# Kernel optimization log

Hardware: AMD Instinct MI355X
Metric: run time of the kernel (lower is better)

## Reference

```python
import jax, jax.numpy as jnp
import numpy as np

MARGIN = 1.0   # TripletLoss(margin) init arg
EPS = 1e-6     # torch F.pairwise_distance eps used by nn.TripletMarginLoss
INF = 1e9

N, D_EMB, N_CLASSES = 8192, 1024, 128


def setup_inputs() -> dict:
    key = jax.random.key(0)
    k1, k2 = jax.random.split(key)
    embeddings = jax.random.normal(k1, (N, D_EMB), dtype=jnp.float32)
    target = jax.random.randint(k2, (N,), 0, N_CLASSES, dtype=jnp.int64 if jax.config.jax_enable_x64 else jnp.int32)
    return {"embeddings": embeddings, "target": target}


def _mine_and_loss(embeddings, target):
    # Vectorized, deterministic equivalent of the per-anchor random mining loop:
    # full pairwise L2 distance matrix via a GEMM (compute-bound core).
    sq = jnp.sum(embeddings * embeddings, axis=1)                      # [N]
    d2 = sq[:, None] + sq[None, :] - 2.0 * (embeddings @ embeddings.T)  # [N, N]
    Dm = jnp.sqrt(jnp.maximum(d2, 0.0))                                 # [N, N]

    same = target[:, None] == target[None, :]
    eye = jnp.eye(target.shape[0], dtype=bool)
    pos_mask = same & ~eye          # valid positives (same class, not self)
    neg_mask = ~same                # valid negatives (different class)

    # Positive: hardest (farthest) same-class sample (deterministic stand-in
    # for the original's random positive draw).
    pos_scores = jnp.where(pos_mask, Dm, -INF)
    pos_idx = jnp.argmax(pos_scores, axis=1)                           # [N]
    d_p = jnp.max(pos_scores, axis=1)                                  # [N]

    # Negative: semi-hard (d_p < d_n < d_p + margin), pick the closest such
    # negative; if none exists, fall back to the overall hardest (min-dist)
    # negative -- mirrors the loop's early-break vs. min_dist fallback.
    semi = neg_mask & (Dm > d_p[:, None]) & (Dm < (d_p + MARGIN)[:, None])
    has_semi = jnp.any(semi, axis=1)
    neg_semi = jnp.argmin(jnp.where(semi, Dm, INF), axis=1)
    neg_hard = jnp.argmin(jnp.where(neg_mask, Dm, INF), axis=1)
    neg_idx = jnp.where(has_semi, neg_semi, neg_hard)                  # [N]

    # nn.TripletMarginLoss(margin, p=2): mean(relu(d(a,p) - d(a,n) + margin))
    # with torch's pairwise_distance eps added to the difference.
    a = embeddings
    p = embeddings[pos_idx]
    n = embeddings[neg_idx]
    dp = jnp.sqrt(jnp.sum((a - p + EPS) ** 2, axis=1))
    dn = jnp.sqrt(jnp.sum((a - n + EPS) ** 2, axis=1))
    return jnp.mean(jax.nn.relu(dp - dn + MARGIN))


def reference(embeddings, target):
    return _mine_and_loss(embeddings, target)
```

## Files before the change

kernel.cpp:

```cpp
#include <hip/hip_runtime.h>
#include <hip/hip_bf16.h>

#define N 8192
#define D 1024
#define MARGIN 1.0f
#define EPS 1e-6f

typedef __attribute__((ext_vector_type(8))) short bf16x8;
typedef __attribute__((ext_vector_type(4))) float f32x4;
typedef __attribute__((ext_vector_type(8))) _Float16 f16x8;
typedef __attribute__((ext_vector_type(4))) _Float16 f16x4;
typedef __attribute__((ext_vector_type(8))) unsigned short u16x8;

__device__ inline unsigned short f2bf(float x) {
    unsigned u = __float_as_uint(x);
    unsigned r = (u + 0x7FFFu + ((u >> 16) & 1u)) >> 16;
    return (unsigned short)r;
}

__device__ inline float h2f(unsigned hb) {
    return (float)__builtin_bit_cast(_Float16, (unsigned short)hb);
}

__global__ __launch_bounds__(256) void prep_kernel(const float* __restrict__ E,
                                                   unsigned short* __restrict__ Ebf,
                                                   float* __restrict__ sq) {
    const int r = blockIdx.x;
    const int tid = threadIdx.x;
    const float4 v = ((const float4*)(E + (size_t)r * D))[tid];
    ushort4 o;
    o.x = f2bf(v.x); o.y = f2bf(v.y); o.z = f2bf(v.z); o.w = f2bf(v.w);
    ((ushort4*)(Ebf + (size_t)r * D))[tid] = o;
    float s = v.x * v.x + v.y * v.y + v.z * v.z + v.w * v.w;
    for (int off = 32; off > 0; off >>= 1) s += __shfl_down(s, off);
    __shared__ float red[4];
    const int lane = tid & 63, wave = tid >> 6;
    if (lane == 0) red[wave] = s;
    __syncthreads();
    if (tid == 0) sq[r] = red[0] + red[1] + red[2] + red[3];
}

__global__ __launch_bounds__(256) void cls_kernel(const int* __restrict__ target,
                                                  unsigned char* __restrict__ cls) {
    const int t = blockIdx.x * 256 + threadIdx.x;
    cls[t] = (unsigned char)target[t];
}

__global__ __launch_bounds__(256) void gemm_kernel(const unsigned short* __restrict__ E,
                                                   const float* __restrict__ sq,
                                                   _Float16* __restrict__ D2h) {
    __shared__ char smem[128 * 136 * 2];
    unsigned short* As = (unsigned short*)smem;
    unsigned short* Bs = (unsigned short*)(smem + 8192);
    _Float16* Ts = (_Float16*)smem;

    const int tid = threadIdx.x;
    const int lane = tid & 63;
    const int wave = tid >> 6;
    const int wm = wave & 1, wn = wave >> 1;

    const int l = blockIdx.x;
    int by = (int)((sqrtf(8.0f * (float)l + 1.0f) - 1.0f) * 0.5f);
    while ((by + 1) * (by + 2) / 2 <= l) ++by;
    while (by * (by + 1) / 2 > l) --by;
    const int bx = l - by * (by + 1) / 2;
    const int rm = by * 128;
    const int cn = bx * 128;

    const int srow = tid >> 2;
    const int scol = (tid & 3) * 8;

    const unsigned short* gA = E + (size_t)(rm + srow) * D + scol;
    const unsigned short* gB = E + (size_t)(cn + srow) * D + scol;

    f32x4 acc[4][4] = {};

    const int kq = (lane >> 4) * 8;
    const int mr = lane & 15;

    for (int k0 = 0; k0 < D; k0 += 32) {
        __builtin_amdgcn_global_load_lds(
            (const __attribute__((address_space(1))) unsigned int*)(gA + k0),
            (__attribute__((address_space(3))) unsigned int*)((char*)As + wave * 1024), 16, 0, 0);
        __builtin_amdgcn_global_load_lds(
            (const __attribute__((address_space(1))) unsigned int*)(gA + (size_t)64 * D + k0),
            (__attribute__((address_space(3))) unsigned int*)((char*)As + 4096 + wave * 1024), 16, 0, 0);
        __builtin_amdgcn_global_load_lds(
            (const __attribute__((address_space(1))) unsigned int*)(gB + k0),
            (__attribute__((address_space(3))) unsigned int*)((char*)Bs + wave * 1024), 16, 0, 0);
        __builtin_amdgcn_global_load_lds(
            (const __attribute__((address_space(1))) unsigned int*)(gB + (size_t)64 * D + k0),
            (__attribute__((address_space(3))) unsigned int*)((char*)Bs + 4096 + wave * 1024), 16, 0, 0);
        __syncthreads();

        bf16x8 af[4], bfr[4];
#pragma unroll
        for (int mi = 0; mi < 4; ++mi)
            af[mi] = *(const bf16x8*)(As + (wm * 64 + mi * 16 + mr) * 32 + kq);
#pragma unroll
        for (int ni = 0; ni < 4; ++ni)
            bfr[ni] = *(const bf16x8*)(Bs + (wn * 64 + ni * 16 + mr) * 32 + kq);
#pragma unroll
        for (int mi = 0; mi < 4; ++mi)
#pragma unroll
            for (int ni = 0; ni < 4; ++ni)
                acc[mi][ni] = __builtin_amdgcn_mfma_f32_16x16x32_bf16(af[mi], bfr[ni], acc[mi][ni], 0, 0, 0);
        __syncthreads();
    }

    const int crow = (lane >> 4) * 4;
    const int ccol = lane & 15;
    const bool offdiag = (bx != by);
    float sqj[4];
#pragma unroll
    for (int ni = 0; ni < 4; ++ni)
        sqj[ni] = sq[cn + wn * 64 + ni * 16 + ccol];
#pragma unroll
    for (int mi = 0; mi < 4; ++mi) {
        const int lrow = wm * 64 + mi * 16 + crow;
        const int i0 = rm + lrow;
        float sqi[4];
#pragma unroll
        for (int r = 0; r < 4; ++r) sqi[r] = sq[i0 + r];
#pragma unroll
        for (int ni = 0; ni < 4; ++ni) {
            const int lcol = wn * 64 + ni * 16 + ccol;
            const int j = cn + lcol;
            f16x4 tv;
#pragma unroll
            for (int r = 0; r < 4; ++r) {
                float d2 = fmaxf(sqi[r] + sqj[ni] - 2.0f * acc[mi][ni][r], 0.0f);
                _Float16 h = (_Float16)d2;
                D2h[(size_t)(i0 + r) * N + j] = h;
                tv[r] = h;
            }
            if (offdiag)
                *(f16x4*)(Ts + (size_t)lcol * 136 + lrow) = tv;
        }
    }
    if (offdiag) {
        __syncthreads();
#pragma unroll
        for (int it = 0; it < 8; ++it) {
            const int rt = it * 16 + (tid >> 4);
            const int seg = tid & 15;
            f16x8 v = *(const f16x8*)(Ts + (size_t)rt * 136 + seg * 8);
            *(f16x8*)(D2h + (size_t)(cn + rt) * N + rm + seg * 8) = v;
        }
    }
}

__global__ __launch_bounds__(256) void mine_kernel(const _Float16* __restrict__ D2h,
                                                   const unsigned char* __restrict__ cls,
                                                   float* __restrict__ loss_arr) {
    const int i = blockIdx.x;
    const int tid = threadIdx.x;
    const int lane = tid & 63, wave = tid >> 6;
    const unsigned tcb = cls[i];
    const unsigned short* row = (const unsigned short*)(D2h + (size_t)i * N);

    u16x8 v[4];
    unsigned long long c8[4];
#pragma unroll
    for (int it = 0; it < 4; ++it) {
        v[it] = *(const u16x8*)(row + it * 2048 + tid * 8);
        c8[it] = *(const unsigned long long*)(cls + it * 2048 + tid * 8);
    }

    unsigned pm = 0u, nm = 0xFFFFu;
#pragma unroll
    for (int it = 0; it < 4; ++it) {
#pragma unroll
        for (int e = 0; e < 8; ++e) {
            const unsigned hb = v[it][e];
            const bool s = ((unsigned)(c8[it] >> (8 * e)) & 0xFFu) == tcb;
            pm = max(pm, s ? hb : 0u);
            nm = min(nm, s ? 0xFFFFu : hb);
        }
    }
    for (int off = 1; off < 64; off <<= 1) {
        pm = max(pm, (unsigned)__shfl_xor((int)pm, off));
        nm = min(nm, (unsigned)__shfl_xor((int)nm, off));
    }
    __shared__ unsigned redp[4], redn[4], reds[4];
    if (lane == 0) { redp[wave] = pm; redn[wave] = nm; }
    __syncthreads();
    pm = max(max(redp[0], redp[1]), max(redp[2], redp[3]));
    nm = min(min(redn[0], redn[1]), min(redn[2], redn[3]));
    const unsigned lob = pm;

    unsigned sm = 0xFFFFu;
#pragma unroll
    for (int it = 0; it < 4; ++it) {
#pragma unroll
        for (int e = 0; e < 8; ++e) {
            const unsigned hb = v[it][e];
            sm = min(sm, hb > lob ? hb : 0xFFFFu);
        }
    }
    for (int off = 1; off < 64; off <<= 1)
        sm = min(sm, (unsigned)__shfl_xor((int)sm, off));
    if (lane == 0) reds[wave] = sm;
    __syncthreads();
    if (tid == 0) {
        sm = min(min(reds[0], reds[1]), min(reds[2], reds[3]));
        const float lo = h2f(lob);
        const float dp = sqrtf(lo);
        const float hw = dp + MARGIN;
        const float hi = hw * hw;
        const float smv = h2f(sm);
        const float dn2 = (smv < hi) ? smv : h2f(nm);
        loss_arr[i] = fmaxf(dp - sqrtf(dn2) + MARGIN, 0.0f);
    }
}

__global__ __launch_bounds__(256) void reduce_kernel(const float* __restrict__ loss_arr,
                                                     float* __restrict__ out) {
    const int tid = threadIdx.x;
    float s = 0.0f;
    for (int k = tid; k < N; k += 256) s += loss_arr[k];
    for (int off = 32; off > 0; off >>= 1) s += __shfl_down(s, off);
    __shared__ float red[4];
    const int lane = tid & 63, wave = tid >> 6;
    if (lane == 0) red[wave] = s;
    __syncthreads();
    if (tid == 0) out[0] = (red[0] + red[1] + red[2] + red[3]) * (1.0f / N);
}

extern "C" void kernel_launch(void* const* d_in, const int* in_sizes, int n_in,
                              void* d_out, int out_size, void* d_ws, size_t ws_size,
                              hipStream_t stream) {
    const float* E = (const float*)d_in[0];
    const int* target = (const int*)d_in[1];
    float* out = (float*)d_out;
    char* ws = (char*)d_ws;

    unsigned short* Ebf = (unsigned short*)ws;
    float* sq        = (float*)(ws + (size_t)16777216);
    float* loss_arr  = (float*)(ws + (size_t)16809984);
    unsigned char* cls = (unsigned char*)(ws + (size_t)16842752);
    _Float16* D2h    = (_Float16*)(ws + (size_t)16875520);

    prep_kernel<<<N, 256, 0, stream>>>(E, Ebf, sq);
    cls_kernel<<<N / 256, 256, 0, stream>>>(target, cls);
    gemm_kernel<<<2080, 256, 0, stream>>>(Ebf, sq, D2h);
    mine_kernel<<<N, 256, 0, stream>>>(D2h, cls, loss_arr);
    reduce_kernel<<<1, 256, 0, stream>>>(loss_arr, out);
}
```

Before: 207.6 us.

## Store only upper-triangle distance tiles and mine rows and columns per tile

The GEMM now writes each symmetric 128x128 distance tile once (its transposed copy only), so the mirrored half of the fp16 distance matrix is never stored. Mining is restructured into tile-based kernels that reduce both row-wise and column-wise within each stored tile. Per-tile partial max/min values go to Ppart/Npart/Spart buffers and are folded by small kernels. A second tile pass then finds the semi-hard negative. The target-to-class conversion is also merged into the prep kernel. The aim is to halve the GEMM's store traffic and rely on symmetry during mining. The cost is two extra launches, partial-buffer traffic, and two reads of the half matrix, with strided column reductions in LDS.

```diff
diff --git a/kernel.cpp b/kernel.cpp
--- a/kernel.cpp
+++ b/kernel.cpp
@@ -5,12 +5,14 @@
 #define D 1024
 #define MARGIN 1.0f
 #define EPS 1e-6f
+#define TSTR 132
 
 typedef __attribute__((ext_vector_type(8))) short bf16x8;
 typedef __attribute__((ext_vector_type(4))) float f32x4;
 typedef __attribute__((ext_vector_type(8))) _Float16 f16x8;
 typedef __attribute__((ext_vector_type(4))) _Float16 f16x4;
 typedef __attribute__((ext_vector_type(8))) unsigned short u16x8;
+typedef __attribute__((ext_vector_type(4))) unsigned short u16x4;
 
 __device__ inline unsigned short f2bf(float x) {
     unsigned u = __float_as_uint(x);
@@ -22,11 +24,25 @@
     return (float)__builtin_bit_cast(_Float16, (unsigned short)hb);
 }
 
+__device__ inline void tri_decode(int l, int& a, int& b) {
+    int bb = (int)((sqrtf(8.0f * (float)l + 1.0f) - 1.0f) * 0.5f);
+    while ((bb + 1) * (bb + 2) / 2 <= l) ++bb;
+    while (bb * (bb + 1) / 2 > l) --bb;
+    b = bb;
+    a = l - bb * (bb + 1) / 2;
+}
+
 __global__ __launch_bounds__(256) void prep_kernel(const float* __restrict__ E,
+                                                   const int* __restrict__ target,
                                                    unsigned short* __restrict__ Ebf,
-                                                   float* __restrict__ sq) {
+                                                   float* __restrict__ sq,
+                                                   unsigned char* __restrict__ cls) {
     const int r = blockIdx.x;
     const int tid = threadIdx.x;
+    if (r < 32) {
+        const int idx = r * 256 + tid;
+        cls[idx] = (unsigned char)target[idx];
+    }
     const float4 v = ((const float4*)(E + (size_t)r * D))[tid];
     ushort4 o;
     o.x = f2bf(v.x); o.y = f2bf(v.y); o.z = f2bf(v.z); o.w = f2bf(v.w);
@@ -40,16 +56,10 @@
     if (tid == 0) sq[r] = red[0] + red[1] + red[2] + red[3];
 }
 
-__global__ __launch_bounds__(256) void cls_kernel(const int* __restrict__ target,
-                                                  unsigned char* __restrict__ cls) {
-    const int t = blockIdx.x * 256 + threadIdx.x;
-    cls[t] = (unsigned char)target[t];
-}
-
 __global__ __launch_bounds__(256) void gemm_kernel(const unsigned short* __restrict__ E,
                                                    const float* __restrict__ sq,
                                                    _Float16* __restrict__ D2h) {
-    __shared__ char smem[128 * 136 * 2];
+    __shared__ char smem[128 * TSTR * 2];
     unsigned short* As = (unsigned short*)smem;
     unsigned short* Bs = (unsigned short*)(smem + 8192);
     _Float16* Ts = (_Float16*)smem;
@@ -59,11 +69,8 @@
     const int wave = tid >> 6;
     const int wm = wave & 1, wn = wave >> 1;
 
-    const int l = blockIdx.x;
-    int by = (int)((sqrtf(8.0f * (float)l + 1.0f) - 1.0f) * 0.5f);
-    while ((by + 1) * (by + 2) / 2 <= l) ++by;
-    while (by * (by + 1) / 2 > l) --by;
-    const int bx = l - by * (by + 1) / 2;
+    int bx, by;
+    tri_decode(blockIdx.x, bx, by);
     const int rm = by * 128;
     const int cn = bx * 128;
 
@@ -110,7 +117,6 @@
 
     const int crow = (lane >> 4) * 4;
     const int ccol = lane & 15;
-    const bool offdiag = (bx != by);
     float sqj[4];
 #pragma unroll
     for (int ni = 0; ni < 4; ++ni)
@@ -125,93 +131,198 @@
 #pragma unroll
         for (int ni = 0; ni < 4; ++ni) {
             const int lcol = wn * 64 + ni * 16 + ccol;
-            const int j = cn + lcol;
             f16x4 tv;
 #pragma unroll
             for (int r = 0; r < 4; ++r) {
                 float d2 = fmaxf(sqi[r] + sqj[ni] - 2.0f * acc[mi][ni][r], 0.0f);
-                _Float16 h = (_Float16)d2;
-                D2h[(size_t)(i0 + r) * N + j] = h;
-                tv[r] = h;
+                tv[r] = (_Float16)d2;
             }
-            if (offdiag)
-                *(f16x4*)(Ts + (size_t)lcol * 136 + lrow) = tv;
-        }
-    }
-    if (offdiag) {
-        __syncthreads();
-#pragma unroll
-        for (int it = 0; it < 8; ++it) {
-            const int rt = it * 16 + (tid >> 4);
-            const int seg = tid & 15;
-            f16x8 v = *(const f16x8*)(Ts + (size_t)rt * 136 + seg * 8);
-            *(f16x8*)(D2h + (size_t)(cn + rt) * N + rm + seg * 8) = v;
-        }
-    }
-}
-
-__global__ __launch_bounds__(256) void mine_kernel(const _Float16* __restrict__ D2h,
-                                                   const unsigned char* __restrict__ cls,
-                                                   float* __restrict__ loss_arr) {
-    const int i = blockIdx.x;
-    const int tid = threadIdx.x;
-    const int lane = tid & 63, wave = tid >> 6;
-    const unsigned tcb = cls[i];
-    const unsigned short* row = (const unsigned short*)(D2h + (size_t)i * N);
-
-    u16x8 v[4];
-    unsigned long long c8[4];
-#pragma unroll
-    for (int it = 0; it < 4; ++it) {
-        v[it] = *(const u16x8*)(row + it * 2048 + tid * 8);
-        c8[it] = *(const unsigned long long*)(cls + it * 2048 + tid * 8);
-    }
-
-    unsigned pm = 0u, nm = 0xFFFFu;
-#pragma unroll
-    for (int it = 0; it < 4; ++it) {
-#pragma unroll
-        for (int e = 0; e < 8; ++e) {
-            const unsigned hb = v[it][e];
-            const bool s = ((unsigned)(c8[it] >> (8 * e)) & 0xFFu) == tcb;
+            *(f16x4*)(Ts + (size_t)lcol * TSTR + lrow) = tv;
+        }
+    }
+    __syncthreads();
+#pragma unroll
+    for (int it = 0; it < 8; ++it) {
+        const int rt = it * 16 + (tid >> 4);
+        const int seg = tid & 15;
+        f16x4 v0 = *(const f16x4*)(Ts + (size_t)rt * TSTR + seg * 8);
+        f16x4 v1 = *(const f16x4*)(Ts + (size_t)rt * TSTR + seg * 8 + 4);
+        f16x8 v = __builtin_shufflevector(v0, v1, 0, 1, 2, 3, 4, 5, 6, 7);
+        *(f16x8*)(D2h + (size_t)(cn + rt) * N + rm + seg * 8) = v;
+    }
+}
+
+__global__ __launch_bounds__(256) void mineA_kernel(const _Float16* __restrict__ D2h,
+                                                    const unsigned char* __restrict__ cls,
+                                                    unsigned short* __restrict__ Ppart,
+                                                    unsigned short* __restrict__ Npart) {
+    __shared__ unsigned short tile[128 * TSTR];
+    __shared__ unsigned char clsA[128], clsB[128];
+    __shared__ unsigned rpm[256], rnm[256];
+    const int tid = threadIdx.x;
+    int a, b;
+    tri_decode(blockIdx.x, a, b);
+
+    if (tid < 128) clsA[tid] = cls[a * 128 + tid];
+    else           clsB[tid - 128] = cls[b * 128 + (tid - 128)];
+
+    const unsigned short* g = (const unsigned short*)D2h + (size_t)(a * 128) * N + b * 128;
+#pragma unroll
+    for (int it = 0; it < 8; ++it) {
+        const int q = it * 256 + tid;
+        const int r = q >> 4, seg = q & 15;
+        u16x8 v = *(const u16x8*)(g + (size_t)r * N + seg * 8);
+        *(u16x4*)(tile + r * TSTR + seg * 8)     = __builtin_shufflevector(v, v, 0, 1, 2, 3);
+        *(u16x4*)(tile + r * TSTR + seg * 8 + 4) = __builtin_shufflevector(v, v, 4, 5, 6, 7);
+    }
+    __syncthreads();
+
+    {
+        const int r = tid >> 1, half = tid & 1;
+        const unsigned rc = clsA[r];
+        const unsigned short* rowp = tile + r * TSTR + half * 64;
+        const unsigned char* cb = clsB + half * 64;
+        unsigned pm = 0u, nm = 0xFFFFu;
+#pragma unroll
+        for (int k = 0; k < 16; ++k) {
+            u16x4 v = *(const u16x4*)(rowp + k * 4);
+            unsigned c4 = *(const unsigned*)(cb + k * 4);
+#pragma unroll
+            for (int e = 0; e < 4; ++e) {
+                const unsigned hb = v[e];
+                const bool s = ((c4 >> (8 * e)) & 0xFFu) == rc;
+                pm = max(pm, s ? hb : 0u);
+                nm = min(nm, s ? 0xFFFFu : hb);
+            }
+        }
+        rpm[tid] = pm; rnm[tid] = nm;
+    }
+    __syncthreads();
+    if (tid < 128) {
+        const unsigned pm = max(rpm[2 * tid], rpm[2 * tid + 1]);
+        const unsigned nm = min(rnm[2 * tid], rnm[2 * tid + 1]);
+        Ppart[(size_t)b * N + a * 128 + tid] = (unsigned short)pm;
+        Npart[(size_t)b * N + a * 128 + tid] = (unsigned short)nm;
+    }
+
+    if (a != b) {
+        __syncthreads();
+        const int c = tid & 127, rh = tid >> 7;
+        const unsigned cc = clsB[c];
+        unsigned pm = 0u, nm = 0xFFFFu;
+#pragma unroll 8
+        for (int k = 0; k < 64; ++k) {
+            const int rr = rh * 64 + k;
+            const unsigned hb = tile[rr * TSTR + c];
+            const bool s = (clsA[rr] == cc);
             pm = max(pm, s ? hb : 0u);
             nm = min(nm, s ? 0xFFFFu : hb);
         }
-    }
-    for (int off = 1; off < 64; off <<= 1) {
-        pm = max(pm, (unsigned)__shfl_xor((int)pm, off));
-        nm = min(nm, (unsigned)__shfl_xor((int)nm, off));
-    }
-    __shared__ unsigned redp[4], redn[4], reds[4];
-    if (lane == 0) { redp[wave] = pm; redn[wave] = nm; }
-    __syncthreads();
-    pm = max(max(redp[0], redp[1]), max(redp[2], redp[3]));
-    nm = min(min(redn[0], redn[1]), min(redn[2], redn[3]));
-    const unsigned lob = pm;
-
+        rpm[tid] = pm; rnm[tid] = nm;
+        __syncthreads();
+        if (tid < 128) {
+            const unsigned pmc = max(rpm[tid], rpm[tid + 128]);
+            const unsigned nmc = min(rnm[tid], rnm[tid + 128]);
+            Ppart[(size_t)a * N + b * 128 + tid] = (unsigned short)pmc;
+            Npart[(size_t)a * N + b * 128 + tid] = (unsigned short)nmc;
+        }
+    }
+}
+
+__global__ __launch_bounds__(256) void foldA_kernel(const unsigned short* __restrict__ Ppart,
+                                                    const unsigned short* __restrict__ Npart,
+                                                    unsigned short* __restrict__ lob,
+                                                    unsigned short* __restrict__ nmb) {
+    const int i = blockIdx.x * 256 + threadIdx.x;
+    unsigned pm = 0u, nm = 0xFFFFu;
+#pragma unroll 8
+    for (int s = 0; s < 64; ++s) {
+        pm = max(pm, (unsigned)Ppart[(size_t)s * N + i]);
+        nm = min(nm, (unsigned)Npart[(size_t)s * N + i]);
+    }
+    lob[i] = (unsigned short)pm;
+    nmb[i] = (unsigned short)nm;
+}
+
+__global__ __launch_bounds__(256) void mineB_kernel(const _Float16* __restrict__ D2h,
+                                                    const unsigned short* __restrict__ lob,
+                                                    unsigned short* __restrict__ Spart) {
+    __shared__ unsigned short tile[128 * TSTR];
+    __shared__ unsigned short lobA[128], lobB[128];
+    __shared__ unsigned rsm[256];
+    const int tid = threadIdx.x;
+    int a, b;
+    tri_decode(blockIdx.x, a, b);
+
+    if (tid < 128) lobA[tid] = lob[a * 128 + tid];
+    else           lobB[tid - 128] = lob[b * 128 + (tid - 128)];
+
+    const unsigned short* g = (const unsigned short*)D2h + (size_t)(a * 128) * N + b * 128;
+#pragma unroll
+    for (int it = 0; it < 8; ++it) {
+        const int q = it * 256 + tid;
+        const int r = q >> 4, seg = q & 15;
+        u16x8 v = *(const u16x8*)(g + (size_t)r * N + seg * 8);
+        *(u16x4*)(tile + r * TSTR + seg * 8)     = __builtin_shufflevector(v, v, 0, 1, 2, 3);
+        *(u16x4*)(tile + r * TSTR + seg * 8 + 4) = __builtin_shufflevector(v, v, 4, 5, 6, 7);
+    }
+    __syncthreads();
+
+    {
+        const int r = tid >> 1, half = tid & 1;
+        const unsigned lr = lobA[r];
+        const unsigned short* rowp = tile + r * TSTR + half * 64;
+        unsigned sm = 0xFFFFu;
+#pragma unroll
+        for (int k = 0; k < 16; ++k) {
+            u16x4 v = *(const u16x4*)(rowp + k * 4);
+#pragma unroll
+            for (int e = 0; e < 4; ++e) {
+                const unsigned hb = v[e];
+                sm = min(sm, hb > lr ? hb : 0xFFFFu);
+            }
+        }
+        rsm[tid] = sm;
+    }
+    __syncthreads();
+    if (tid < 128)
+        Spart[(size_t)b * N + a * 128 + tid] =
+            (unsigned short)min(rsm[2 * tid], rsm[2 * tid + 1]);
+
+    if (a != b) {
+        __syncthreads();
+        const int c = tid & 127, rh = tid >> 7;
+        const unsigned lc = lobB[c];
+        unsigned sm = 0xFFFFu;
+#pragma unroll 8
+        for (int k = 0; k < 64; ++k) {
+            const unsigned hb = tile[(rh * 64 + k) * TSTR + c];
+            sm = min(sm, hb > lc ? hb : 0xFFFFu);
+        }
+        rsm[tid] = sm;
+        __syncthreads();
+        if (tid < 128)
+            Spart[(size_t)a * N + b * 128 + tid] =
+                (unsigned short)min(rsm[tid], rsm[tid + 128]);
+    }
+}
+
+__global__ __launch_bounds__(256) void foldB_kernel(const unsigned short* __restrict__ Spart,
+                                                    const unsigned short* __restrict__ lob,
+                                                    const unsigned short* __restrict__ nmb,
+                                                    float* __restrict__ loss_arr) {
+    const int i = blockIdx.x * 256 + threadIdx.x;
     unsigned sm = 0xFFFFu;
-#pragma unroll
-    for (int it = 0; it < 4; ++it) {
-#pragma unroll
-        for (int e = 0; e < 8; ++e) {
-            const unsigned hb = v[it][e];
-            sm = min(sm, hb > lob ? hb : 0xFFFFu);
-        }
-    }
-    for (int off = 1; off < 64; off <<= 1)
-        sm = min(sm, (unsigned)__shfl_xor((int)sm, off));
-    if (lane == 0) reds[wave] = sm;
-    __syncthreads();
-    if (tid == 0) {
-        sm = min(min(reds[0], reds[1]), min(reds[2], reds[3]));
-        const float lo = h2f(lob);
-        const float dp = sqrtf(lo);
-        const float hw = dp + MARGIN;
-        const float hi = hw * hw;
-        const float smv = h2f(sm);
-        const float dn2 = (smv < hi) ? smv : h2f(nm);
-        loss_arr[i] = fmaxf(dp - sqrtf(dn2) + MARGIN, 0.0f);
-    }
+#pragma unroll 8
+    for (int s = 0; s < 64; ++s)
+        sm = min(sm, (unsigned)Spart[(size_t)s * N + i]);
+    const float lo = h2f(lob[i]);
+    const float dp = sqrtf(lo);
+    const float hw = dp + MARGIN;
+    const float hi = hw * hw;
+    const float smv = h2f(sm);
+    const float dn2 = (smv < hi) ? smv : h2f(nmb[i]);
+    loss_arr[i] = fmaxf(dp - sqrtf(dn2) + MARGIN, 0.0f);
 }
 
 __global__ __launch_bounds__(256) void reduce_kernel(const float* __restrict__ loss_arr,
@@ -235,15 +346,22 @@
     float* out = (float*)d_out;
     char* ws = (char*)d_ws;
 
-    unsigned short* Ebf = (unsigned short*)ws;
-    float* sq        = (float*)(ws + (size_t)16777216);
-    float* loss_arr  = (float*)(ws + (size_t)16809984);
-    unsigned char* cls = (unsigned char*)(ws + (size_t)16842752);
-    _Float16* D2h    = (_Float16*)(ws + (size_t)16875520);
-
-    prep_kernel<<<N, 256, 0, stream>>>(E, Ebf, sq);
-    cls_kernel<<<N / 256, 256, 0, stream>>>(target, cls);
+    unsigned short* Ebf   = (unsigned short*)ws;
+    float* sq             = (float*)(ws + (size_t)16777216);
+    float* loss_arr       = (float*)(ws + (size_t)16809984);
+    unsigned char* cls    = (unsigned char*)(ws + (size_t)16842752);
+    unsigned short* lob   = (unsigned short*)(ws + (size_t)16875520);
+    unsigned short* nmb   = (unsigned short*)(ws + (size_t)16908288);
+    unsigned short* Ppart = (unsigned short*)(ws + (size_t)16941056);
+    unsigned short* Npart = (unsigned short*)(ws + (size_t)17989632);
+    unsigned short* Spart = (unsigned short*)(ws + (size_t)19038208);
+    _Float16* D2h         = (_Float16*)(ws + (size_t)20086784);
+
+    prep_kernel<<<N, 256, 0, stream>>>(E, target, Ebf, sq, cls);
     gemm_kernel<<<2080, 256, 0, stream>>>(Ebf, sq, D2h);
-    mine_kernel<<<N, 256, 0, stream>>>(D2h, cls, loss_arr);
+    mineA_kernel<<<2080, 256, 0, stream>>>(D2h, cls, Ppart, Npart);
+    foldA_kernel<<<N / 256, 256, 0, stream>>>(Ppart, Npart, lob, nmb);
+    mineB_kernel<<<2080, 256, 0, stream>>>(D2h, lob, Spart);
+    foldB_kernel<<<N / 256, 256, 0, stream>>>(Spart, lob, nmb, loss_arr);
     reduce_kernel<<<1, 256, 0, stream>>>(loss_arr, out);
 }
```

Result: slower. 211.7 us (+2.0%).

## Store only upper-triangle distance tiles and mine rows/columns per tile with atomics

Applied to the files above, without the earlier changes.

The GEMM now writes each symmetric tile once instead of twice, and mining is restructured into two tile-based passes over the triangle. Each pass reduces both row and column extrema and combines them through global atomicMax/atomicMin. This halves distance-matrix write traffic. It also adds an LDS swizzle for the GEMM operand reads and fuses the cls/initialisation work into prep and the final mean into an atomic fold. The cost is atomic contention and a second pass over the stored half-matrix.

```diff
diff --git a/kernel.cpp b/kernel.cpp
--- a/kernel.cpp
+++ b/kernel.cpp
@@ -4,7 +4,7 @@
 #define N 8192
 #define D 1024
 #define MARGIN 1.0f
-#define EPS 1e-6f
+#define TSTR 132
 
 typedef __attribute__((ext_vector_type(8))) short bf16x8;
 typedef __attribute__((ext_vector_type(4))) float f32x4;
@@ -19,14 +19,36 @@
 }
 
 __device__ inline float h2f(unsigned hb) {
-    return (float)__builtin_bit_cast(_Float16, (unsigned short)hb);
+    return (float)__builtin_bit_cast(_Float16, (unsigned short)(hb & 0xFFFFu));
+}
+
+__device__ inline void tri_decode(int l, int& a, int& b) {
+    int bb = (int)((sqrtf(8.0f * (float)l + 1.0f) - 1.0f) * 0.5f);
+    while ((bb + 1) * (bb + 2) / 2 <= l) ++bb;
+    while (bb * (bb + 1) / 2 > l) --bb;
+    b = bb;
+    a = l - bb * (bb + 1) / 2;
 }
 
 __global__ __launch_bounds__(256) void prep_kernel(const float* __restrict__ E,
+                                                   const int* __restrict__ target,
                                                    unsigned short* __restrict__ Ebf,
-                                                   float* __restrict__ sq) {
+                                                   float* __restrict__ sq,
+                                                   unsigned char* __restrict__ cls,
+                                                   unsigned* __restrict__ P,
+                                                   unsigned* __restrict__ Nn,
+                                                   unsigned* __restrict__ S,
+                                                   float* __restrict__ out) {
     const int r = blockIdx.x;
     const int tid = threadIdx.x;
+    if (r < 32) {
+        const int idx = r * 256 + tid;
+        cls[idx] = (unsigned char)target[idx];
+        P[idx] = 0u;
+        Nn[idx] = 0xFFFFFFFFu;
+        S[idx] = 0xFFFFFFFFu;
+        if (idx == 0) out[0] = 0.0f;
+    }
     const float4 v = ((const float4*)(E + (size_t)r * D))[tid];
     ushort4 o;
     o.x = f2bf(v.x); o.y = f2bf(v.y); o.z = f2bf(v.z); o.w = f2bf(v.w);
@@ -40,16 +62,10 @@
     if (tid == 0) sq[r] = red[0] + red[1] + red[2] + red[3];
 }
 
-__global__ __launch_bounds__(256) void cls_kernel(const int* __restrict__ target,
-                                                  unsigned char* __restrict__ cls) {
-    const int t = blockIdx.x * 256 + threadIdx.x;
-    cls[t] = (unsigned char)target[t];
-}
-
 __global__ __launch_bounds__(256) void gemm_kernel(const unsigned short* __restrict__ E,
                                                    const float* __restrict__ sq,
                                                    _Float16* __restrict__ D2h) {
-    __shared__ char smem[128 * 136 * 2];
+    __shared__ char smem[128 * TSTR * 2];
     unsigned short* As = (unsigned short*)smem;
     unsigned short* Bs = (unsigned short*)(smem + 8192);
     _Float16* Ts = (_Float16*)smem;
@@ -59,24 +75,22 @@
     const int wave = tid >> 6;
     const int wm = wave & 1, wn = wave >> 1;
 
-    const int l = blockIdx.x;
-    int by = (int)((sqrtf(8.0f * (float)l + 1.0f) - 1.0f) * 0.5f);
-    while ((by + 1) * (by + 2) / 2 <= l) ++by;
-    while (by * (by + 1) / 2 > l) --by;
-    const int bx = l - by * (by + 1) / 2;
+    int bx, by;
+    tri_decode(blockIdx.x, bx, by);
     const int rm = by * 128;
     const int cn = bx * 128;
 
     const int srow = tid >> 2;
-    const int scol = (tid & 3) * 8;
+    const int rot_s = (srow >> 1) & 3;
+    const int scol = (((tid & 3) + rot_s) & 3) * 8;
 
     const unsigned short* gA = E + (size_t)(rm + srow) * D + scol;
     const unsigned short* gB = E + (size_t)(cn + srow) * D + scol;
 
     f32x4 acc[4][4] = {};
 
-    const int kq = (lane >> 4) * 8;
     const int mr = lane & 15;
+    const int kq2 = ((((lane >> 4)) - ((mr >> 1) & 3)) & 3) * 8;
 
     for (int k0 = 0; k0 < D; k0 += 32) {
         __builtin_amdgcn_global_load_lds(
@@ -96,10 +110,10 @@
         bf16x8 af[4], bfr[4];
 #pragma unroll
         for (int mi = 0; mi < 4; ++mi)
-            af[mi] = *(const bf16x8*)(As + (wm * 64 + mi * 16 + mr) * 32 + kq);
+            af[mi] = *(const bf16x8*)(As + (wm * 64 + mi * 16 + mr) * 32 + kq2);
 #pragma unroll
         for (int ni = 0; ni < 4; ++ni)
-            bfr[ni] = *(const bf16x8*)(Bs + (wn * 64 + ni * 16 + mr) * 32 + kq);
+            bfr[ni] = *(const bf16x8*)(Bs + (wn * 64 + ni * 16 + mr) * 32 + kq2);
 #pragma unroll
         for (int mi = 0; mi < 4; ++mi)
 #pragma unroll
@@ -110,7 +124,6 @@
 
     const int crow = (lane >> 4) * 4;
     const int ccol = lane & 15;
-    const bool offdiag = (bx != by);
     float sqj[4];
 #pragma unroll
     for (int ni = 0; ni < 4; ++ni)
@@ -125,106 +138,188 @@
 #pragma unroll
         for (int ni = 0; ni < 4; ++ni) {
             const int lcol = wn * 64 + ni * 16 + ccol;
-            const int j = cn + lcol;
             f16x4 tv;
 #pragma unroll
             for (int r = 0; r < 4; ++r) {
                 float d2 = fmaxf(sqi[r] + sqj[ni] - 2.0f * acc[mi][ni][r], 0.0f);
-                _Float16 h = (_Float16)d2;
-                D2h[(size_t)(i0 + r) * N + j] = h;
-                tv[r] = h;
+                tv[r] = (_Float16)d2;
             }
-            if (offdiag)
-                *(f16x4*)(Ts + (size_t)lcol * 136 + lrow) = tv;
+            *(f16x4*)(Ts + (size_t)lcol * TSTR + lrow) = tv;
+        }
+    }
+    __syncthreads();
+#pragma unroll
+    for (int it = 0; it < 8; ++it) {
+        const int rt = it * 16 + (tid >> 4);
+        const int seg = tid & 15;
+        f16x4 v0 = *(const f16x4*)(Ts + (size_t)rt * TSTR + seg * 8);
+        f16x4 v1 = *(const f16x4*)(Ts + (size_t)rt * TSTR + seg * 8 + 4);
+        f16x8 v = __builtin_shufflevector(v0, v1, 0, 1, 2, 3, 4, 5, 6, 7);
+        *(f16x8*)(D2h + (size_t)(cn + rt) * N + rm + seg * 8) = v;
+    }
+}
+
+__global__ __launch_bounds__(256) void mineA_kernel(const _Float16* __restrict__ D2h,
+                                                    const unsigned char* __restrict__ cls,
+                                                    unsigned* __restrict__ P,
+                                                    unsigned* __restrict__ Nn) {
+    __shared__ unsigned char clsA_l[128], clsB_l[128];
+    __shared__ unsigned short colP_l[4][128], colN_l[4][128];
+    const int tid = threadIdx.x;
+    const int lane = tid & 63, wave = tid >> 6;
+    int a, b;
+    tri_decode(blockIdx.x, a, b);
+    if (tid < 128) clsA_l[tid] = cls[a * 128 + tid];
+    else           clsB_l[tid - 128] = cls[b * 128 + (tid - 128)];
+    __syncthreads();
+
+    const int cg = tid & 15;
+    const int rg = tid >> 4;
+    const unsigned long long c8 = *(const unsigned long long*)(clsB_l + cg * 8);
+    const unsigned short* g = (const unsigned short*)D2h + (size_t)(a * 128) * N + b * 128 + cg * 8;
+    const bool offdiag = (a != b);
+
+    unsigned cp[8], cnn[8];
+#pragma unroll
+    for (int e = 0; e < 8; ++e) { cp[e] = 0u; cnn[e] = 0xFFFFu; }
+
+#pragma unroll
+    for (int k = 0; k < 8; ++k) {
+        const int r = k * 16 + rg;
+        const unsigned rc = clsA_l[r];
+        const u16x8 v = *(const u16x8*)(g + (size_t)r * N);
+        unsigned rp = 0u, rn = 0xFFFFu;
+#pragma unroll
+        for (int e = 0; e < 8; ++e) {
+            const unsigned hb = v[e];
+            const bool s = (((unsigned)(c8 >> (8 * e)) & 0xFFu) == rc);
+            rp = max(rp, s ? hb : 0u);
+            rn = min(rn, s ? 0xFFFFu : hb);
+            cp[e] = max(cp[e], s ? hb : 0u);
+            cnn[e] = min(cnn[e], s ? 0xFFFFu : hb);
+        }
+#pragma unroll
+        for (int m = 1; m < 16; m <<= 1) {
+            rp = max(rp, (unsigned)__shfl_xor((int)rp, m));
+            rn = min(rn, (unsigned)__shfl_xor((int)rn, m));
+        }
+        if (cg == 0) {
+            atomicMax(&P[a * 128 + r], rp);
+            atomicMin(&Nn[a * 128 + r], rn);
         }
     }
     if (offdiag) {
+#pragma unroll
+        for (int e = 0; e < 8; ++e) {
+#pragma unroll
+            for (int m = 16; m < 64; m <<= 1) {
+                cp[e] = max(cp[e], (unsigned)__shfl_xor((int)cp[e], m));
+                cnn[e] = min(cnn[e], (unsigned)__shfl_xor((int)cnn[e], m));
+            }
+        }
+        if (lane < 16) {
+#pragma unroll
+            for (int e = 0; e < 8; ++e) {
+                colP_l[wave][cg * 8 + e] = (unsigned short)cp[e];
+                colN_l[wave][cg * 8 + e] = (unsigned short)cnn[e];
+            }
+        }
         __syncthreads();
-#pragma unroll
-        for (int it = 0; it < 8; ++it) {
-            const int rt = it * 16 + (tid >> 4);
-            const int seg = tid & 15;
-            f16x8 v = *(const f16x8*)(Ts + (size_t)rt * 136 + seg * 8);
-            *(f16x8*)(D2h + (size_t)(cn + rt) * N + rm + seg * 8) = v;
-        }
-    }
-}
-
-__global__ __launch_bounds__(256) void mine_kernel(const _Float16* __restrict__ D2h,
-                                                   const unsigned char* __restrict__ cls,
-                                                   float* __restrict__ loss_arr) {
-    const int i = blockIdx.x;
+        if (tid < 128) {
+            const unsigned pm = max(max((unsigned)colP_l[0][tid], (unsigned)colP_l[1][tid]),
+                                    max((unsigned)colP_l[2][tid], (unsigned)colP_l[3][tid]));
+            const unsigned nm = min(min((unsigned)colN_l[0][tid], (unsigned)colN_l[1][tid]),
+                                    min((unsigned)colN_l[2][tid], (unsigned)colN_l[3][tid]));
+            atomicMax(&P[b * 128 + tid], pm);
+            atomicMin(&Nn[b * 128 + tid], nm);
+        }
+    }
+}
+
+__global__ __launch_bounds__(256) void mineB_kernel(const _Float16* __restrict__ D2h,
+                                                    const unsigned* __restrict__ P,
+                                                    unsigned* __restrict__ S) {
+    __shared__ unsigned short lobA_l[128], lobB_l[128];
+    __shared__ unsigned short colS_l[4][128];
     const int tid = threadIdx.x;
     const int lane = tid & 63, wave = tid >> 6;
-    const unsigned tcb = cls[i];
-    const unsigned short* row = (const unsigned short*)(D2h + (size_t)i * N);
-
-    u16x8 v[4];
-    unsigned long long c8[4];
-#pragma unroll
-    for (int it = 0; it < 4; ++it) {
-        v[it] = *(const u16x8*)(row + it * 2048 + tid * 8);
-        c8[it] = *(const unsigned long long*)(cls + it * 2048 + tid * 8);
-    }
-
-    unsigned pm = 0u, nm = 0xFFFFu;
-#pragma unroll
-    for (int it = 0; it < 4; ++it) {
+    int a, b;
+    tri_decode(blockIdx.x, a, b);
+    if (tid < 128) lobA_l[tid] = (unsigned short)P[a * 128 + tid];
+    else           lobB_l[tid - 128] = (unsigned short)P[b * 128 + (tid - 128)];
+    __syncthreads();
+
+    const int cg = tid & 15;
+    const int rg = tid >> 4;
+    unsigned lb[8];
+#pragma unroll
+    for (int e = 0; e < 8; ++e) lb[e] = lobB_l[cg * 8 + e];
+    const unsigned short* g = (const unsigned short*)D2h + (size_t)(a * 128) * N + b * 128 + cg * 8;
+    const bool offdiag = (a != b);
+
+    unsigned sc[8];
+#pragma unroll
+    for (int e = 0; e < 8; ++e) sc[e] = 0xFFFFu;
+
+#pragma unroll
+    for (int k = 0; k < 8; ++k) {
+        const int r = k * 16 + rg;
+        const unsigned lr = lobA_l[r];
+        const u16x8 v = *(const u16x8*)(g + (size_t)r * N);
+        unsigned sr = 0xFFFFu;
 #pragma unroll
         for (int e = 0; e < 8; ++e) {
-            const unsigned hb = v[it][e];
-            const bool s = ((unsigned)(c8[it] >> (8 * e)) & 0xFFu) == tcb;
-            pm = max(pm, s ? hb : 0u);
-            nm = min(nm, s ? 0xFFFFu : hb);
-        }
-    }
-    for (int off = 1; off < 64; off <<= 1) {
-        pm = max(pm, (unsigned)__shfl_xor((int)pm, off));
-        nm = min(nm, (unsigned)__shfl_xor((int)nm, off));
-    }
-    __shared__ unsigned redp[4], redn[4], reds[4];
-    if (lane == 0) { redp[wave] = pm; redn[wave] = nm; }
-    __syncthreads();
-    pm = max(max(redp[0], redp[1]), max(redp[2], redp[3]));
-    nm = min(min(redn[0], redn[1]), min(redn[2], redn[3]));
-    const unsigned lob = pm;
-
-    unsigned sm = 0xFFFFu;
-#pragma unroll
-    for (int it = 0; it < 4; ++it) {
+            const unsigned hb = v[e];
+            sr = min(sr, hb > lr ? hb : 0xFFFFu);
+            sc[e] = min(sc[e], hb > lb[e] ? hb : 0xFFFFu);
+        }
+#pragma unroll
+        for (int m = 1; m < 16; m <<= 1)
+            sr = min(sr, (unsigned)__shfl_xor((int)sr, m));
+        if (cg == 0)
+            atomicMin(&S[a * 128 + r], sr);
+    }
+    if (offdiag) {
 #pragma unroll
         for (int e = 0; e < 8; ++e) {
-            const unsigned hb = v[it][e];
-            sm = min(sm, hb > lob ? hb : 0xFFFFu);
-        }
-    }
-    for (int off = 1; off < 64; off <<= 1)
-        sm = min(sm, (unsigned)__shfl_xor((int)sm, off));
-    if (lane == 0) reds[wave] = sm;
-    __syncthreads();
-    if (tid == 0) {
-        sm = min(min(reds[0], reds[1]), min(reds[2], reds[3]));
-        const float lo = h2f(lob);
-        const float dp = sqrtf(lo);
-        const float hw = dp + MARGIN;
-        const float hi = hw * hw;
-        const float smv = h2f(sm);
-        const float dn2 = (smv < hi) ? smv : h2f(nm);
-        loss_arr[i] = fmaxf(dp - sqrtf(dn2) + MARGIN, 0.0f);
-    }
-}
-
-__global__ __launch_bounds__(256) void reduce_kernel(const float* __restrict__ loss_arr,
-                                                     float* __restrict__ out) {
-    const int tid = threadIdx.x;
-    float s = 0.0f;
-    for (int k = tid; k < N; k += 256) s += loss_arr[k];
-    for (int off = 32; off > 0; off >>= 1) s += __shfl_down(s, off);
+#pragma unroll
+            for (int m = 16; m < 64; m <<= 1)
+                sc[e] = min(sc[e], (unsigned)__shfl_xor((int)sc[e], m));
+        }
+        if (lane < 16) {
+#pragma unroll
+            for (int e = 0; e < 8; ++e)
+                colS_l[wave][cg * 8 + e] = (unsigned short)sc[e];
+        }
+        __syncthreads();
+        if (tid < 128) {
+            const unsigned sm = min(min((unsigned)colS_l[0][tid], (unsigned)colS_l[1][tid]),
+                                    min((unsigned)colS_l[2][tid], (unsigned)colS_l[3][tid]));
+            atomicMin(&S[b * 128 + tid], sm);
+        }
+    }
+}
+
+__global__ __launch_bounds__(256) void foldB_kernel(const unsigned* __restrict__ P,
+                                                    const unsigned* __restrict__ Nn,
+                                                    const unsigned* __restrict__ S,
+                                                    float* __restrict__ out) {
+    const int tid = threadIdx.x;
+    const int i = blockIdx.x * 256 + tid;
+    const float lo = h2f(P[i]);
+    const float dp = sqrtf(lo);
+    const float hw = dp + MARGIN;
+    const float hi = hw * hw;
+    const float smv = h2f(S[i]);
+    const float dn2 = (smv < hi) ? smv : h2f(Nn[i]);
+    float loss = fmaxf(dp - sqrtf(dn2) + MARGIN, 0.0f);
+    for (int off = 32; off > 0; off >>= 1) loss += __shfl_down(loss, off);
     __shared__ float red[4];
     const int lane = tid & 63, wave = tid >> 6;
-    if (lane == 0) red[wave] = s;
-    __syncthreads();
-    if (tid == 0) out[0] = (red[0] + red[1] + red[2] + red[3]) * (1.0f / N);
+    if (lane == 0) red[wave] = loss;
+    __syncthreads();
+    if (tid == 0)
+        atomicAdd(out, (red[0] + red[1] + red[2] + red[3]) * (1.0f / N));
 }
 
 extern "C" void kernel_launch(void* const* d_in, const int* in_sizes, int n_in,
@@ -236,14 +331,16 @@
     char* ws = (char*)d_ws;
 
     unsigned short* Ebf = (unsigned short*)ws;
-    float* sq        = (float*)(ws + (size_t)16777216);
-    float* loss_arr  = (float*)(ws + (size_t)16809984);
-    unsigned char* cls = (unsigned char*)(ws + (size_t)16842752);
-    _Float16* D2h    = (_Float16*)(ws + (size_t)16875520);
-
-    prep_kernel<<<N, 256, 0, stream>>>(E, Ebf, sq);
-    cls_kernel<<<N / 256, 256, 0, stream>>>(target, cls);
+    float* sq           = (float*)(ws + (size_t)16777216);
+    unsigned char* cls  = (unsigned char*)(ws + (size_t)16809984);
+    unsigned* P         = (unsigned*)(ws + (size_t)16842752);
+    unsigned* Nn        = (unsigned*)(ws + (size_t)16875520);
+    unsigned* S         = (unsigned*)(ws + (size_t)16908288);
+    _Float16* D2h       = (_Float16*)(ws + (size_t)16941056);
+
+    prep_kernel<<<N, 256, 0, stream>>>(E, target, Ebf, sq, cls, P, Nn, S, out);
     gemm_kernel<<<2080, 256, 0, stream>>>(Ebf, sq, D2h);
-    mine_kernel<<<N, 256, 0, stream>>>(D2h, cls, loss_arr);
-    reduce_kernel<<<1, 256, 0, stream>>>(loss_arr, out);
-}
+    mineA_kernel<<<2080, 256, 0, stream>>>(D2h, cls, P, Nn);
+    mineB_kernel<<<2080, 256, 0, stream>>>(D2h, P, S);
+    foldB_kernel<<<N / 256, 256, 0, stream>>>(P, Nn, S, out);
+}
```

After: 212.1 us. +2.2%, slower.
